# Performance work log

Hardware: AMD Instinct MI355X
Metric: run time of the kernel (lower is better)

The kernel has to match this reference:

```python
import jax, jax.numpy as jnp
import numpy as np

B, S, F = 8, 2048, 1024
NEG = -1000000000.0

def setup_inputs() -> dict:
    key = jax.random.key(0)
    ks = jax.random.split(key, 8)
    x = jax.random.normal(ks[0], (B, S, F), dtype=jnp.float32)
    # causal attention mask [S, S], 1 = keep, 0 = masked
    attn_mask = jnp.tril(jnp.ones((S, S), dtype=jnp.int32))
    # key padding mask [B, 1, S], random 0/1
    pad_mask = jax.random.randint(ks[1], (B, 1, S), 0, 2, dtype=jnp.int32)
    # ensure at least the first key position is valid per batch to avoid all-masked rows
    pad_mask = pad_mask.at[:, :, 0].set(1)
    sc = 1.0 / np.sqrt(F).astype(np.float32)
    Wq = jax.random.normal(ks[2], (F, F), dtype=jnp.float32) * sc
    bq = jax.random.normal(ks[3], (F,), dtype=jnp.float32) * 0.01
    Wk = jax.random.normal(ks[4], (F, F), dtype=jnp.float32) * sc
    bk = jax.random.normal(ks[5], (F,), dtype=jnp.float32) * 0.01
    Wv = jax.random.normal(ks[6], (F, F), dtype=jnp.float32) * sc
    bv = jax.random.normal(ks[7], (F,), dtype=jnp.float32) * 0.01
    return {"x": x, "attn_mask": attn_mask, "pad_mask": pad_mask,
            "Wq": Wq, "bq": bq, "Wk": Wk, "bk": bk, "Wv": Wv, "bv": bv}

def reference(x, attn_mask, pad_mask, Wq, bq, Wk, bk, Wv, bv):
    # torch Linear: y = x @ W.T + b
    q = jnp.einsum('bsf,of->bso', x, Wq) + bq
    k = jnp.einsum('bsf,of->bso', x, Wk) + bk
    v = jnp.einsum('bsf,of->bso', x, Wv) + bv
    scale = 1.0 / jnp.sqrt(jnp.asarray(q.shape[-1], dtype=x.dtype))
    scores = jnp.einsum('bqf,bkf->bqk', q, k) * scale  # [B, S, S]
    scores = jnp.where(pad_mask == 0, NEG, scores)            # pad_mask [B,1,S] broadcasts
    scores = jnp.where(attn_mask[None, :, :] == 0, NEG, scores)
    prob = jax.nn.softmax(scores, axis=-1)
    # dropout=0.0 (eval / identity)
    return jnp.einsum('bqk,bkf->bqf', prob, v)
```

## Files before the change

kernel.cpp:

```cpp
#include <hip/hip_runtime.h>
#include <hip/hip_bf16.h>
#include <stdint.h>


#define S_LEN 2048
#define F_DIM 1024
#define NBATCH 8
#define BS_TOT (NBATCH * S_LEN)

typedef __attribute__((ext_vector_type(8))) short bf16x8;
typedef __attribute__((ext_vector_type(4))) float f32x4;
typedef unsigned short u16;

__device__ __forceinline__ u16 f32_to_bf16_rne(float f) {
    union { float f; uint32_t u; } v; v.f = f;
    uint32_t u = v.u;
    u += 0x7FFFu + ((u >> 16) & 1u);
    return (u16)(u >> 16);
}
__device__ __forceinline__ float bf16_to_f32(u16 h) {
    union { uint32_t u; float f; } v; v.u = ((uint32_t)h) << 16;
    return v.f;
}

__device__ __forceinline__ void gload_lds16(const u16* g, u16* l) {
    __builtin_amdgcn_global_load_lds(
        (const __attribute__((address_space(1))) void*)g,
        (__attribute__((address_space(3))) void*)l,
        16, 0, 0);
}

__global__ __launch_bounds__(256) void cvt_f32_bf16(const float* __restrict__ in,
                                                    u16* __restrict__ out, int n) {
    int i = (blockIdx.x * 256 + threadIdx.x) * 4;
    if (i + 3 < n) {
        float4 f = *(const float4*)(in + i);
        ushort4 o;
        o.x = f32_to_bf16_rne(f.x); o.y = f32_to_bf16_rne(f.y);
        o.z = f32_to_bf16_rne(f.z); o.w = f32_to_bf16_rne(f.w);
        *(ushort4*)(out + i) = o;
    }
}

__global__ __launch_bounds__(256) void cvt_w3(const float* __restrict__ Wq,
                                              const float* __restrict__ Wk,
                                              const float* __restrict__ Wv,
                                              u16* __restrict__ Wb) {
    const int which = blockIdx.y;
    const float* in = (which == 0) ? Wq : (which == 1) ? Wk : Wv;
    int i = (blockIdx.x * 256 + threadIdx.x) * 4;
    float4 f = *(const float4*)(in + i);
    ushort4 o;
    o.x = f32_to_bf16_rne(f.x); o.y = f32_to_bf16_rne(f.y);
    o.z = f32_to_bf16_rne(f.z); o.w = f32_to_bf16_rne(f.w);
    *(ushort4*)(Wb + (size_t)which * F_DIM * F_DIM + i) = o;
}

__global__ __launch_bounds__(256) void k_scan(const int* __restrict__ pad,
                                              int* __restrict__ cidx,
                                              int* __restrict__ sIdx,
                                              int* __restrict__ kneed) {
    const int b = blockIdx.x;
    const int tid = threadIdx.x;
    const int* p = pad + b * S_LEN;
    __shared__ int part[256];
    __shared__ int cnt_s;
    int v[8]; int sum = 0; const int s0 = tid * 8;
#pragma unroll
    for (int i = 0; i < 8; i++) { v[i] = p[s0 + i]; sum += v[i]; }
    part[tid] = sum;
    __syncthreads();
    if (tid == 0) {
        int acc = 0;
        for (int i = 0; i < 256; i++) { int t = part[i]; part[i] = acc; acc += t; }
        cnt_s = acc;
    }
    __syncthreads();
    int run = part[tid];
#pragma unroll
    for (int i = 0; i < 8; i++) {
        const int s = s0 + i;
        cidx[b * S_LEN + s] = run;
        if (v[i]) sIdx[b * S_LEN + run] = s;
        run += v[i];
    }
    const int cnt = cnt_s;
    for (int c = cnt + tid; c < S_LEN; c += 256) sIdx[b * S_LEN + c] = S_LEN;
    if (tid < 16) {
        const int et = (tid + 1) * 16 - 1;
        kneed[b * 16 + tid] = (et == 255) ? cnt : part[et + 1];
    }
}

template<class Epi>
__device__ __forceinline__ void gemm_tile_128(
    const u16* __restrict__ A, int lda,
    const u16* __restrict__ Bt, int ldb,
    int m0, int n0, int K, float alpha, Epi epi)
{
    __shared__ u16 la[128 * 32];
    __shared__ u16 lb[128 * 32];

    const int tid  = threadIdx.x;
    const int lane = tid & 63;
    const int wave = tid >> 6;
    const int wm = (wave & 1) * 64;
    const int wn = (wave >> 1) * 64;

    f32x4 acc[4][4];
#pragma unroll
    for (int mt = 0; mt < 4; mt++)
#pragma unroll
        for (int nt = 0; nt < 4; nt++)
            acc[mt][nt] = f32x4{0.f, 0.f, 0.f, 0.f};

    const int mrow = wm + (lane & 15);
    const int nrow = wn + (lane & 15);
    const int koff = (lane >> 4) * 8;

    const int cb0 = wave * 64;
    const int cb1 = wave * 64 + 256;
    const int lrow = lane >> 2;
    const int lcol = (lane & 3) * 8;
    const u16* pa0 = A  + (size_t)(m0 + (cb0 >> 2) + lrow) * lda + lcol;
    const u16* pa1 = A  + (size_t)(m0 + (cb1 >> 2) + lrow) * lda + lcol;
    const u16* pb0 = Bt + (size_t)(n0 + (cb0 >> 2) + lrow) * ldb + lcol;
    const u16* pb1 = Bt + (size_t)(n0 + (cb1 >> 2) + lrow) * ldb + lcol;
    u16* qa0 = la + cb0 * 8;
    u16* qa1 = la + cb1 * 8;
    u16* qb0 = lb + cb0 * 8;
    u16* qb1 = lb + cb1 * 8;

    for (int kk = 0; kk < K; kk += 32) {
        __syncthreads();
        gload_lds16(pa0 + kk, qa0);
        gload_lds16(pa1 + kk, qa1);
        gload_lds16(pb0 + kk, qb0);
        gload_lds16(pb1 + kk, qb1);
        __syncthreads();

        bf16x8 fa[4], fb[4];
#pragma unroll
        for (int t = 0; t < 4; t++) {
            fa[t] = *(const bf16x8*)(la + (mrow + t * 16) * 32 + koff);
            fb[t] = *(const bf16x8*)(lb + (nrow + t * 16) * 32 + koff);
        }
#pragma unroll
        for (int mt = 0; mt < 4; mt++)
#pragma unroll
            for (int nt = 0; nt < 4; nt++)
                acc[mt][nt] = __builtin_amdgcn_mfma_f32_16x16x32_bf16(
                    fa[mt], fb[nt], acc[mt][nt], 0, 0, 0);
    }

    const int col   = lane & 15;
    const int rquad = (lane >> 4) * 4;
#pragma unroll
    for (int mt = 0; mt < 4; mt++)
#pragma unroll
        for (int nt = 0; nt < 4; nt++) {
            const int n = n0 + wn + nt * 16 + col;
#pragma unroll
            for (int r = 0; r < 4; r++) {
                const int m = m0 + wm + mt * 16 + rquad + r;
                epi(m, n, acc[mt][nt][r] * alpha);
            }
        }
}

__global__ __launch_bounds__(256) void k_qkv(const u16* __restrict__ xb,
                                             const u16* __restrict__ Wb,
                                             const float* __restrict__ bq,
                                             const float* __restrict__ bk,
                                             const float* __restrict__ bv,
                                             const int* __restrict__ pad,
                                             const int* __restrict__ cidx,
                                             u16* __restrict__ q,
                                             u16* __restrict__ kc,
                                             u16* __restrict__ vTc) {
    const int which = blockIdx.y;
    const int bx = blockIdx.x;
    const int xcd = bx & 7;
    const int idx = bx >> 3;
    const int m0 = (xcd * 16 + (idx >> 3)) * 128;
    const int n0 = (idx & 7) * 128;
    const float* bias = (which == 0) ? bq : (which == 1) ? bk : bv;
    const u16* W = Wb + (size_t)which * F_DIM * F_DIM;
    if (which == 0) {
        gemm_tile_128(xb, F_DIM, W, F_DIM, m0, n0, F_DIM, 1.0f,
            [&](int m, int n, float v) {
                q[(size_t)m * F_DIM + n] = f32_to_bf16_rne(v + bias[n]);
            });
    } else if (which == 1) {
        gemm_tile_128(xb, F_DIM, W, F_DIM, m0, n0, F_DIM, 1.0f,
            [&](int m, int n, float v) {
                const int b = m >> 11, s = m & 2047;
                if (pad[b * S_LEN + s])
                    kc[((size_t)b * S_LEN + cidx[b * S_LEN + s]) * F_DIM + n] =
                        f32_to_bf16_rne(v + bias[n]);
            });
    } else {
        gemm_tile_128(xb, F_DIM, W, F_DIM, m0, n0, F_DIM, 1.0f,
            [&](int m, int n, float v) {
                const int b = m >> 11, s = m & 2047;
                if (pad[b * S_LEN + s])
                    vTc[((size_t)b * F_DIM + n) * S_LEN + cidx[b * S_LEN + s]] =
                        f32_to_bf16_rne(v + bias[n]);
            });
    }
}

__global__ __launch_bounds__(256) void k_scores(const u16* __restrict__ q,
                                                const u16* __restrict__ kc,
                                                const int* __restrict__ sIdx,
                                                const int* __restrict__ kneed,
                                                u16* __restrict__ Pp,
                                                float* __restrict__ lsum) {
    const int b = blockIdx.x & 7;
    const int t = blockIdx.x >> 3;
    int it = 0, base = 0;
    while (base + it + 1 <= t) { base += it + 1; it++; }
    const int jt = t - base;
    if (jt * 128 >= kneed[b * 16 + it]) return;
    const int* sIb = sIdx + b * S_LEN;
    u16* Pb = Pp + (size_t)b * S_LEN * S_LEN;

    float rs[16];
#pragma unroll
    for (int i = 0; i < 16; i++) rs[i] = 0.f;

    gemm_tile_128(q + (size_t)b * S_LEN * F_DIM, F_DIM,
                  kc + (size_t)b * S_LEN * F_DIM, F_DIM,
                  it * 128, jt * 128, F_DIM, 0.03125f,
        [&](int m, int n, float v) {
            u16 o = 0;
            if (sIb[n] <= m)
                o = f32_to_bf16_rne(__expf(v - 16.0f));
            Pb[(size_t)m * S_LEN + n] = o;
            const int i = m & 63;
            rs[((i >> 4) << 2) | (i & 3)] += bf16_to_f32(o);
        });

    const int lane  = threadIdx.x & 63;
    const int wave  = threadIdx.x >> 6;
    const int wm    = (wave & 1) * 64;
    const int rquad = (lane >> 4) * 4;
    float* lb = lsum + b * S_LEN + it * 128 + wm;
#pragma unroll
    for (int i = 0; i < 16; i++) {
        float s = rs[i];
        s += __shfl_xor(s, 1);
        s += __shfl_xor(s, 2);
        s += __shfl_xor(s, 4);
        s += __shfl_xor(s, 8);
        if ((lane & 15) == 0)
            atomicAdd(&lb[((i >> 2) << 4) + rquad + (i & 3)], s);
    }
}

__global__ __launch_bounds__(256) void k_pv(const u16* __restrict__ Pp,
                                            const u16* __restrict__ vTc,
                                            const float* __restrict__ lsum,
                                            const int* __restrict__ kneed,
                                            float* __restrict__ out) {
    const int b = blockIdx.x & 7;
    const int rest = blockIdx.x >> 3;
    const int j = rest >> 3;
    const int nt = rest & 7;
    const int it = (j & 1) ? (j >> 1) : (15 - (j >> 1));
    const int Keff = (kneed[b * 16 + it] + 127) & ~127;
    const float* ls = lsum + b * S_LEN;
    float* ob = out + (size_t)b * S_LEN * F_DIM;

    const int lane  = threadIdx.x & 63;
    const int wave  = threadIdx.x >> 6;
    const int wm    = (wave & 1) * 64;
    const int rquad = (lane >> 4) * 4;
    const int mb    = it * 128 + wm;
    float myinv[16];
#pragma unroll
    for (int i = 0; i < 16; i++)
        myinv[i] = 1.0f / ls[mb + ((i >> 2) << 4) + rquad + (i & 3)];

    gemm_tile_128(Pp + (size_t)b * S_LEN * S_LEN, S_LEN,
                  vTc + (size_t)b * F_DIM * S_LEN, S_LEN,
                  it * 128, nt * 128, Keff, 1.0f,
        [&](int m, int n, float v) {
            const int i = m & 63;
            ob[(size_t)m * F_DIM + n] = v * myinv[((i >> 4) << 2) | (i & 3)];
        });
}

extern "C" void kernel_launch(void* const* d_in, const int* in_sizes, int n_in,
                              void* d_out, int out_size, void* d_ws, size_t ws_size,
                              hipStream_t stream) {
    const float* x  = (const float*)d_in[0];
    const int* pad  = (const int*)d_in[2];
    const float* Wq = (const float*)d_in[3];
    const float* bq = (const float*)d_in[4];
    const float* Wk = (const float*)d_in[5];
    const float* bk = (const float*)d_in[6];
    const float* Wv = (const float*)d_in[7];
    const float* bv = (const float*)d_in[8];
    float* out = (float*)d_out;

    char* ws = (char*)d_ws;
    u16* q    = (u16*)(ws);
    u16* kc   = (u16*)(ws + 32ull * 1024 * 1024);
    u16* vTc  = (u16*)(ws + 64ull * 1024 * 1024);
    u16* Pp   = (u16*)(ws + 96ull * 1024 * 1024);
    u16* xb   = (u16*)(ws + 160ull * 1024 * 1024);
    u16* Wb   = (u16*)(ws + 192ull * 1024 * 1024);
    float* il = (float*)(ws + 200ull * 1024 * 1024);
    int* cidx = (int*)(ws + 201ull * 1024 * 1024);
    int* sIdx = (int*)(ws + 202ull * 1024 * 1024);
    int* kneed= (int*)(ws + 203ull * 1024 * 1024);

    const int BSF = BS_TOT * F_DIM;
    const int FF = F_DIM * F_DIM;

    hipMemsetAsync(il, 0, BS_TOT * sizeof(float), stream);
    hipMemsetAsync(vTc, 0, 32ull * 1024 * 1024, stream);

    cvt_f32_bf16<<<BSF / 1024, 256, 0, stream>>>(x, xb, BSF);
    cvt_w3<<<dim3(FF / 1024, 3), 256, 0, stream>>>(Wq, Wk, Wv, Wb);
    k_scan<<<NBATCH, 256, 0, stream>>>(pad, cidx, sIdx, kneed);

    k_qkv<<<dim3(1024, 3), 256, 0, stream>>>(xb, Wb, bq, bk, bv, pad, cidx,
                                             q, kc, vTc);

    k_scores<<<1088, 256, 0, stream>>>(q, kc, sIdx, kneed, Pp, il);

    k_pv<<<1024, 256, 0, stream>>>(Pp, vTc, il, kneed, out);
}
```

Baseline: 386.5 us.

## Use 128x64 tiles for scores and PV, merge pad/index lookup in QKV epilogue

Adds a 128x64 GEMM tile variant and uses it for the scores and P·V kernels, doubling the grid sizes and rounding the per-row key extent to 64 instead of 128. This lets the compacted key range skip more padded columns and gives more blocks for occupancy, at the cost of less operand reuse per tile. The scan now writes a single destination index (-1 when padded), so the K/V epilogue makes one lookup instead of reading both pad and cidx, and the three QKV branches are merged into one lambda.

```diff
diff --git a/kernel.cpp b/kernel.cpp
--- a/kernel.cpp
+++ b/kernel.cpp
@@ -57,7 +57,7 @@
 }
 
 __global__ __launch_bounds__(256) void k_scan(const int* __restrict__ pad,
-                                              int* __restrict__ cidx,
+                                              int* __restrict__ dstc,
                                               int* __restrict__ sIdx,
                                               int* __restrict__ kneed) {
     const int b = blockIdx.x;
@@ -80,7 +80,7 @@
 #pragma unroll
     for (int i = 0; i < 8; i++) {
         const int s = s0 + i;
-        cidx[b * S_LEN + s] = run;
+        dstc[b * S_LEN + s] = v[i] ? run : -1;
         if (v[i]) sIdx[b * S_LEN + run] = s;
         run += v[i];
     }
@@ -168,13 +168,86 @@
         }
 }
 
+template<class Epi>
+__device__ __forceinline__ void gemm_tile_64n(
+    const u16* __restrict__ A, int lda,
+    const u16* __restrict__ Bt, int ldb,
+    int m0, int n0, int K, float alpha, Epi epi)
+{
+    __shared__ u16 la[128 * 32];
+    __shared__ u16 lb[64 * 32];
+
+    const int tid  = threadIdx.x;
+    const int lane = tid & 63;
+    const int wave = tid >> 6;
+    const int wm = (wave & 1) * 64;
+    const int wn = (wave >> 1) * 32;
+
+    f32x4 acc[4][2];
+#pragma unroll
+    for (int mt = 0; mt < 4; mt++)
+#pragma unroll
+        for (int nt = 0; nt < 2; nt++)
+            acc[mt][nt] = f32x4{0.f, 0.f, 0.f, 0.f};
+
+    const int mrow = wm + (lane & 15);
+    const int nrow = wn + (lane & 15);
+    const int koff = (lane >> 4) * 8;
+
+    const int cb0 = wave * 64;
+    const int cb1 = wave * 64 + 256;
+    const int lrow = lane >> 2;
+    const int lcol = (lane & 3) * 8;
+    const u16* pa0 = A  + (size_t)(m0 + (cb0 >> 2) + lrow) * lda + lcol;
+    const u16* pa1 = A  + (size_t)(m0 + (cb1 >> 2) + lrow) * lda + lcol;
+    const u16* pb0 = Bt + (size_t)(n0 + (cb0 >> 2) + lrow) * ldb + lcol;
+    u16* qa0 = la + cb0 * 8;
+    u16* qa1 = la + cb1 * 8;
+    u16* qb0 = lb + cb0 * 8;
+
+    for (int kk = 0; kk < K; kk += 32) {
+        __syncthreads();
+        gload_lds16(pa0 + kk, qa0);
+        gload_lds16(pa1 + kk, qa1);
+        gload_lds16(pb0 + kk, qb0);
+        __syncthreads();
+
+        bf16x8 fa[4], fb[2];
+#pragma unroll
+        for (int t = 0; t < 4; t++)
+            fa[t] = *(const bf16x8*)(la + (mrow + t * 16) * 32 + koff);
+#pragma unroll
+        for (int t = 0; t < 2; t++)
+            fb[t] = *(const bf16x8*)(lb + (nrow + t * 16) * 32 + koff);
+#pragma unroll
+        for (int mt = 0; mt < 4; mt++)
+#pragma unroll
+            for (int nt = 0; nt < 2; nt++)
+                acc[mt][nt] = __builtin_amdgcn_mfma_f32_16x16x32_bf16(
+                    fa[mt], fb[nt], acc[mt][nt], 0, 0, 0);
+    }
+
+    const int col   = lane & 15;
+    const int rquad = (lane >> 4) * 4;
+#pragma unroll
+    for (int mt = 0; mt < 4; mt++)
+#pragma unroll
+        for (int nt = 0; nt < 2; nt++) {
+            const int n = n0 + wn + nt * 16 + col;
+#pragma unroll
+            for (int r = 0; r < 4; r++) {
+                const int m = m0 + wm + mt * 16 + rquad + r;
+                epi(m, n, acc[mt][nt][r] * alpha);
+            }
+        }
+}
+
 __global__ __launch_bounds__(256) void k_qkv(const u16* __restrict__ xb,
                                              const u16* __restrict__ Wb,
                                              const float* __restrict__ bq,
                                              const float* __restrict__ bk,
                                              const float* __restrict__ bv,
-                                             const int* __restrict__ pad,
-                                             const int* __restrict__ cidx,
+                                             const int* __restrict__ dstc,
                                              u16* __restrict__ q,
                                              u16* __restrict__ kc,
                                              u16* __restrict__ vTc) {
@@ -184,30 +257,25 @@
     const int idx = bx >> 3;
     const int m0 = (xcd * 16 + (idx >> 3)) * 128;
     const int n0 = (idx & 7) * 128;
+    const int b  = m0 >> 11;
     const float* bias = (which == 0) ? bq : (which == 1) ? bk : bv;
     const u16* W = Wb + (size_t)which * F_DIM * F_DIM;
-    if (which == 0) {
-        gemm_tile_128(xb, F_DIM, W, F_DIM, m0, n0, F_DIM, 1.0f,
-            [&](int m, int n, float v) {
-                q[(size_t)m * F_DIM + n] = f32_to_bf16_rne(v + bias[n]);
-            });
-    } else if (which == 1) {
-        gemm_tile_128(xb, F_DIM, W, F_DIM, m0, n0, F_DIM, 1.0f,
-            [&](int m, int n, float v) {
-                const int b = m >> 11, s = m & 2047;
-                if (pad[b * S_LEN + s])
-                    kc[((size_t)b * S_LEN + cidx[b * S_LEN + s]) * F_DIM + n] =
-                        f32_to_bf16_rne(v + bias[n]);
-            });
-    } else {
-        gemm_tile_128(xb, F_DIM, W, F_DIM, m0, n0, F_DIM, 1.0f,
-            [&](int m, int n, float v) {
-                const int b = m >> 11, s = m & 2047;
-                if (pad[b * S_LEN + s])
-                    vTc[((size_t)b * F_DIM + n) * S_LEN + cidx[b * S_LEN + s]] =
-                        f32_to_bf16_rne(v + bias[n]);
-            });
-    }
+    const int* db = dstc + b * S_LEN;
+    gemm_tile_128(xb, F_DIM, W, F_DIM, m0, n0, F_DIM, 1.0f,
+        [&](int m, int n, float v) {
+            const u16 h = f32_to_bf16_rne(v + bias[n]);
+            if (which == 0) {
+                q[(size_t)m * F_DIM + n] = h;
+            } else {
+                const int d = db[m & 2047];
+                if (d >= 0) {
+                    if (which == 1)
+                        kc[((size_t)b * S_LEN + d) * F_DIM + n] = h;
+                    else
+                        vTc[((size_t)b * F_DIM + n) * S_LEN + d] = h;
+                }
+            }
+        });
 }
 
 __global__ __launch_bounds__(256) void k_scores(const u16* __restrict__ q,
@@ -219,9 +287,9 @@
     const int b = blockIdx.x & 7;
     const int t = blockIdx.x >> 3;
     int it = 0, base = 0;
-    while (base + it + 1 <= t) { base += it + 1; it++; }
+    while (base + 2 * it + 2 <= t) { base += 2 * it + 2; it++; }
     const int jt = t - base;
-    if (jt * 128 >= kneed[b * 16 + it]) return;
+    if (jt * 64 >= kneed[b * 16 + it]) return;
     const int* sIb = sIdx + b * S_LEN;
     u16* Pb = Pp + (size_t)b * S_LEN * S_LEN;
 
@@ -229,9 +297,9 @@
 #pragma unroll
     for (int i = 0; i < 16; i++) rs[i] = 0.f;
 
-    gemm_tile_128(q + (size_t)b * S_LEN * F_DIM, F_DIM,
+    gemm_tile_64n(q + (size_t)b * S_LEN * F_DIM, F_DIM,
                   kc + (size_t)b * S_LEN * F_DIM, F_DIM,
-                  it * 128, jt * 128, F_DIM, 0.03125f,
+                  it * 128, jt * 64, F_DIM, 0.03125f,
         [&](int m, int n, float v) {
             u16 o = 0;
             if (sIb[n] <= m)
@@ -265,10 +333,10 @@
                                             float* __restrict__ out) {
     const int b = blockIdx.x & 7;
     const int rest = blockIdx.x >> 3;
-    const int j = rest >> 3;
-    const int nt = rest & 7;
+    const int j = rest >> 4;
+    const int nt = rest & 15;
     const int it = (j & 1) ? (j >> 1) : (15 - (j >> 1));
-    const int Keff = (kneed[b * 16 + it] + 127) & ~127;
+    const int Keff = (kneed[b * 16 + it] + 63) & ~63;
     const float* ls = lsum + b * S_LEN;
     float* ob = out + (size_t)b * S_LEN * F_DIM;
 
@@ -282,9 +350,9 @@
     for (int i = 0; i < 16; i++)
         myinv[i] = 1.0f / ls[mb + ((i >> 2) << 4) + rquad + (i & 3)];
 
-    gemm_tile_128(Pp + (size_t)b * S_LEN * S_LEN, S_LEN,
+    gemm_tile_64n(Pp + (size_t)b * S_LEN * S_LEN, S_LEN,
                   vTc + (size_t)b * F_DIM * S_LEN, S_LEN,
-                  it * 128, nt * 128, Keff, 1.0f,
+                  it * 128, nt * 64, Keff, 1.0f,
         [&](int m, int n, float v) {
             const int i = m & 63;
             ob[(size_t)m * F_DIM + n] = v * myinv[((i >> 4) << 2) | (i & 3)];
@@ -312,7 +380,7 @@
     u16* xb   = (u16*)(ws + 160ull * 1024 * 1024);
     u16* Wb   = (u16*)(ws + 192ull * 1024 * 1024);
     float* il = (float*)(ws + 200ull * 1024 * 1024);
-    int* cidx = (int*)(ws + 201ull * 1024 * 1024);
+    int* dstc = (int*)(ws + 201ull * 1024 * 1024);
     int* sIdx = (int*)(ws + 202ull * 1024 * 1024);
     int* kneed= (int*)(ws + 203ull * 1024 * 1024);
 
@@ -324,12 +392,12 @@
 
     cvt_f32_bf16<<<BSF / 1024, 256, 0, stream>>>(x, xb, BSF);
     cvt_w3<<<dim3(FF / 1024, 3), 256, 0, stream>>>(Wq, Wk, Wv, Wb);
-    k_scan<<<NBATCH, 256, 0, stream>>>(pad, cidx, sIdx, kneed);
-
-    k_qkv<<<dim3(1024, 3), 256, 0, stream>>>(xb, Wb, bq, bk, bv, pad, cidx,
+    k_scan<<<NBATCH, 256, 0, stream>>>(pad, dstc, sIdx, kneed);
+
+    k_qkv<<<dim3(1024, 3), 256, 0, stream>>>(xb, Wb, bq, bk, bv, dstc,
                                              q, kc, vTc);
 
-    k_scores<<<1088, 256, 0, stream>>>(q, kc, sIdx, kneed, Pp, il);
-
-    k_pv<<<1024, 256, 0, stream>>>(Pp, vTc, il, kneed, out);
-}
+    k_scores<<<2176, 256, 0, stream>>>(q, kc, sIdx, kneed, Pp, il);
+
+    k_pv<<<2048, 256, 0, stream>>>(Pp, vTc, il, kneed, out);
+}
```

Measured after the change: 416.4 us. 1.08x slower.

## Gather unpadded rows before K/V projection and skip padded tiles

Applied to the files above, without the earlier changes.

A new gather kernel compacts the bf16 input rows whose key padding is valid into a dense buffer. The K and V projection GEMMs then run on this compacted input and skip tiles past each batch's valid count, so roughly half the K/V GEMM work is avoided. The scattered epilogue stores and the vT memset go away. In exchange the change adds an extra gather kernel launch and a copy pass, and reuses the P buffer region for the compacted input. V tiles still write zeros for rows past the valid count inside a partially filled tile.

```diff
diff --git a/kernel.cpp b/kernel.cpp
--- a/kernel.cpp
+++ b/kernel.cpp
@@ -57,7 +57,6 @@
 }
 
 __global__ __launch_bounds__(256) void k_scan(const int* __restrict__ pad,
-                                              int* __restrict__ cidx,
                                               int* __restrict__ sIdx,
                                               int* __restrict__ kneed) {
     const int b = blockIdx.x;
@@ -80,7 +79,6 @@
 #pragma unroll
     for (int i = 0; i < 8; i++) {
         const int s = s0 + i;
-        cidx[b * S_LEN + s] = run;
         if (v[i]) sIdx[b * S_LEN + run] = s;
         run += v[i];
     }
@@ -90,6 +88,18 @@
         const int et = (tid + 1) * 16 - 1;
         kneed[b * 16 + tid] = (et == 255) ? cnt : part[et + 1];
     }
+}
+
+__global__ __launch_bounds__(256) void k_gather(const u16* __restrict__ xb,
+                                                const int* __restrict__ sIdx,
+                                                const int* __restrict__ kneed,
+                                                u16* __restrict__ xc) {
+    const int b = blockIdx.x >> 11, c = blockIdx.x & 2047;
+    if (c >= kneed[b * 16 + 15]) return;
+    const int s = sIdx[b * S_LEN + c];
+    const ushort4 v = *(const ushort4*)(xb + ((size_t)b * S_LEN + s) * F_DIM
+                                        + threadIdx.x * 4);
+    *(ushort4*)(xc + ((size_t)b * S_LEN + c) * F_DIM + threadIdx.x * 4) = v;
 }
 
 template<class Epi>
@@ -169,12 +179,12 @@
 }
 
 __global__ __launch_bounds__(256) void k_qkv(const u16* __restrict__ xb,
+                                             const u16* __restrict__ xc,
                                              const u16* __restrict__ Wb,
                                              const float* __restrict__ bq,
                                              const float* __restrict__ bk,
                                              const float* __restrict__ bv,
-                                             const int* __restrict__ pad,
-                                             const int* __restrict__ cidx,
+                                             const int* __restrict__ kneed,
                                              u16* __restrict__ q,
                                              u16* __restrict__ kc,
                                              u16* __restrict__ vTc) {
@@ -184,28 +194,24 @@
     const int idx = bx >> 3;
     const int m0 = (xcd * 16 + (idx >> 3)) * 128;
     const int n0 = (idx & 7) * 128;
+    const int b  = m0 >> 11;
+    const int cnt = kneed[b * 16 + 15];
+    if (which > 0 && (m0 & 2047) >= cnt) return;
     const float* bias = (which == 0) ? bq : (which == 1) ? bk : bv;
     const u16* W = Wb + (size_t)which * F_DIM * F_DIM;
-    if (which == 0) {
-        gemm_tile_128(xb, F_DIM, W, F_DIM, m0, n0, F_DIM, 1.0f,
+    const u16* A = (which == 0) ? xb : xc;
+    if (which < 2) {
+        u16* o = (which == 0) ? q : kc;
+        gemm_tile_128(A, F_DIM, W, F_DIM, m0, n0, F_DIM, 1.0f,
             [&](int m, int n, float v) {
-                q[(size_t)m * F_DIM + n] = f32_to_bf16_rne(v + bias[n]);
-            });
-    } else if (which == 1) {
-        gemm_tile_128(xb, F_DIM, W, F_DIM, m0, n0, F_DIM, 1.0f,
-            [&](int m, int n, float v) {
-                const int b = m >> 11, s = m & 2047;
-                if (pad[b * S_LEN + s])
-                    kc[((size_t)b * S_LEN + cidx[b * S_LEN + s]) * F_DIM + n] =
-                        f32_to_bf16_rne(v + bias[n]);
+                o[(size_t)m * F_DIM + n] = f32_to_bf16_rne(v + bias[n]);
             });
     } else {
-        gemm_tile_128(xb, F_DIM, W, F_DIM, m0, n0, F_DIM, 1.0f,
+        gemm_tile_128(A, F_DIM, W, F_DIM, m0, n0, F_DIM, 1.0f,
             [&](int m, int n, float v) {
-                const int b = m >> 11, s = m & 2047;
-                if (pad[b * S_LEN + s])
-                    vTc[((size_t)b * F_DIM + n) * S_LEN + cidx[b * S_LEN + s]] =
-                        f32_to_bf16_rne(v + bias[n]);
+                const int c = m & 2047;
+                vTc[((size_t)b * F_DIM + n) * S_LEN + c] =
+                    (c < cnt) ? f32_to_bf16_rne(v + bias[n]) : (u16)0;
             });
     }
 }
@@ -309,10 +315,10 @@
     u16* kc   = (u16*)(ws + 32ull * 1024 * 1024);
     u16* vTc  = (u16*)(ws + 64ull * 1024 * 1024);
     u16* Pp   = (u16*)(ws + 96ull * 1024 * 1024);
+    u16* xc   = (u16*)(ws + 96ull * 1024 * 1024);
     u16* xb   = (u16*)(ws + 160ull * 1024 * 1024);
     u16* Wb   = (u16*)(ws + 192ull * 1024 * 1024);
     float* il = (float*)(ws + 200ull * 1024 * 1024);
-    int* cidx = (int*)(ws + 201ull * 1024 * 1024);
     int* sIdx = (int*)(ws + 202ull * 1024 * 1024);
     int* kneed= (int*)(ws + 203ull * 1024 * 1024);
 
@@ -320,13 +326,13 @@
     const int FF = F_DIM * F_DIM;
 
     hipMemsetAsync(il, 0, BS_TOT * sizeof(float), stream);
-    hipMemsetAsync(vTc, 0, 32ull * 1024 * 1024, stream);
 
     cvt_f32_bf16<<<BSF / 1024, 256, 0, stream>>>(x, xb, BSF);
     cvt_w3<<<dim3(FF / 1024, 3), 256, 0, stream>>>(Wq, Wk, Wv, Wb);
-    k_scan<<<NBATCH, 256, 0, stream>>>(pad, cidx, sIdx, kneed);
-
-    k_qkv<<<dim3(1024, 3), 256, 0, stream>>>(xb, Wb, bq, bk, bv, pad, cidx,
+    k_scan<<<NBATCH, 256, 0, stream>>>(pad, sIdx, kneed);
+    k_gather<<<BS_TOT, 256, 0, stream>>>(xb, sIdx, kneed, xc);
+
+    k_qkv<<<dim3(1024, 3), 256, 0, stream>>>(xb, xc, Wb, bq, bk, bv, kneed,
                                              q, kc, vTc);
 
     k_scores<<<1088, 256, 0, stream>>>(q, kc, sIdx, kneed, Pp, il);
```

New measurement: 335.3 us. 1.15x faster.
